# Kernel optimization log

Measured on AMD Instinct MI355X. Metric: run time of the kernel, lower is better.

## Reference

```python
import jax, jax.numpy as jnp
import numpy as np

EMBED_DIM = 1024
N_HEADS = 16
HEAD_DIM = EMBED_DIM // N_HEADS
B, S = 4, 2048


def _rope_tables(seq_len, dim):
    inv_freq = 1.0 / (10000.0 ** (jnp.arange(0, dim, 2, dtype=jnp.float32) / dim))
    freqs = jnp.arange(seq_len, dtype=jnp.float32)[:, None] * inv_freq[None, :]  # [S, dim/2]
    return jnp.cos(freqs), jnp.sin(freqs)


def _apply_rope(x, cos, sin):
    # x: [B, H, S, D]; interleaved-pair complex rotation
    x2 = x.reshape(*x.shape[:-1], HEAD_DIM // 2, 2)
    x0, x1 = x2[..., 0], x2[..., 1]
    c = cos[None, None, :, :]
    s = sin[None, None, :, :]
    r0 = x0 * c - x1 * s
    r1 = x0 * s + x1 * c
    return jnp.stack([r0, r1], axis=-1).reshape(x.shape)


def setup_inputs() -> dict:
    key = jax.random.key(0)
    ks = jax.random.split(key, 8)
    sc = 0.02
    return {
        "query": jax.random.normal(ks[0], (B, S, EMBED_DIM), jnp.float32),
        "key": jax.random.normal(ks[1], (B, S, EMBED_DIM), jnp.float32),
        "value": jax.random.normal(ks[2], (B, S, EMBED_DIM), jnp.float32),
        "Wq": jax.random.normal(ks[3], (EMBED_DIM, EMBED_DIM), jnp.float32) * sc,
        "Wk": jax.random.normal(ks[4], (EMBED_DIM, EMBED_DIM), jnp.float32) * sc,
        "Wv": jax.random.normal(ks[5], (EMBED_DIM, EMBED_DIM), jnp.float32) * sc,
        "Wo": jax.random.normal(ks[6], (EMBED_DIM, EMBED_DIM), jnp.float32) * sc,
        "bo": jnp.zeros((EMBED_DIM,), jnp.float32),
    }


def reference(query, key, value, Wq, Wk, Wv, Wo, bo):
    b, s, _ = query.shape
    # torch nn.Linear: y = x @ W.T
    Q = (query @ Wq.T).reshape(b, s, N_HEADS, HEAD_DIM).transpose(0, 2, 1, 3)
    K = (key @ Wk.T).reshape(b, s, N_HEADS, HEAD_DIM).transpose(0, 2, 1, 3)
    V = (value @ Wv.T).reshape(b, s, N_HEADS, HEAD_DIM).transpose(0, 2, 1, 3)
    cos, sin = _rope_tables(s, HEAD_DIM)
    Q = _apply_rope(Q, cos, sin)
    K = _apply_rope(K, cos, sin)
    scores = jnp.einsum("bhqd,bhkd->bhqk", Q, K) / jnp.sqrt(jnp.float32(HEAD_DIM))
    attn = jax.nn.softmax(scores, axis=-1)
    out = jnp.einsum("bhqk,bhkd->bhqd", attn, V)
    out = out.transpose(0, 2, 1, 3).reshape(b, s, EMBED_DIM)
    return out @ Wo.T + bo
```

## Files before the change

kernel.cpp:

```cpp
#include <hip/hip_runtime.h>
#include <math.h>

typedef __attribute__((ext_vector_type(4))) float f32x4;
typedef __attribute__((ext_vector_type(16))) float f32x16;
typedef __attribute__((ext_vector_type(8))) __bf16 bf16x8;
typedef __attribute__((ext_vector_type(4))) unsigned int u32x4;
typedef __attribute__((ext_vector_type(4))) unsigned short u16x4;

#define DEVI __device__ __forceinline__

constexpr size_t WS_WB  = 0;
constexpr size_t WS_COS = 4ull * 1024 * 1024 * 2;
constexpr size_t WS_SIN = WS_COS + 2048 * 32 * 4;
constexpr size_t WS_QH  = WS_SIN + 2048 * 32 * 4;
constexpr size_t WS_KH  = WS_QH + 64ull * 2048 * 64 * 2;
constexpr size_t WS_VT  = WS_KH + 64ull * 2048 * 64 * 2;
constexpr size_t WS_AO  = WS_VT + 64ull * 64 * 2048 * 2;

DEVI unsigned short f2bf(float x) {
  union { float f; unsigned int u; } v; v.f = x;
  unsigned int r = v.u + 0x7fffu + ((v.u >> 16) & 1u);
  return (unsigned short)(r >> 16);
}

DEVI unsigned cvtpk(float a, float b) {
  union { __bf16 h[2]; unsigned u; } x;
  x.h[0] = (__bf16)a; x.h[1] = (__bf16)b;
  return x.u;
}

DEVI void ld_lds16(const void* g, void* l) {
  __builtin_amdgcn_global_load_lds((const __attribute__((address_space(1))) void*)g,
                                   (__attribute__((address_space(3))) void*)l, 16, 0, 0);
}

__global__ __launch_bounds__(256) void prep(const float* __restrict__ w0,
                                            const float* __restrict__ w1,
                                            const float* __restrict__ w2,
                                            const float* __restrict__ w3,
                                            unsigned short* __restrict__ out,
                                            float* __restrict__ cosT,
                                            float* __restrict__ sinT) {
  if (blockIdx.y == 4) {
    if (blockIdx.x >= 256) return;
    int idx = blockIdx.x * 256 + threadIdx.x;
    int s = idx >> 5, i = idx & 31;
    double ang = (double)s * pow(10000.0, -(double)i / 32.0);
    cosT[idx] = (float)cos(ang);
    sinT[idx] = (float)sin(ang);
    return;
  }
  const float* w = blockIdx.y == 0 ? w0 : blockIdx.y == 1 ? w1 : blockIdx.y == 2 ? w2 : w3;
  int i = (blockIdx.x * 256 + threadIdx.x) * 4;
  f32x4 v = *(const f32x4*)(w + i);
  u16x4 o;
  o.x = f2bf(v.x); o.y = f2bf(v.y); o.z = f2bf(v.z); o.w = f2bf(v.w);
  *(u16x4*)(out + (size_t)blockIdx.y * 1048576 + i) = o;
}

__global__ __launch_bounds__(256) void gemm_qkv(const float* __restrict__ Aq,
                                                const float* __restrict__ Ak,
                                                const float* __restrict__ Av,
                                                const unsigned short* __restrict__ Wb,
                                                unsigned short* __restrict__ Qh,
                                                unsigned short* __restrict__ Kh,
                                                unsigned short* __restrict__ Vt,
                                                const float* __restrict__ cosT,
                                                const float* __restrict__ sinT) {
  __shared__ __align__(16) float AsF[128 * 32];
  __shared__ __align__(16) unsigned short Bs[128 * 32];

  const int mat = blockIdx.y;
  const float* A = mat == 0 ? Aq : mat == 1 ? Ak : Av;
  const unsigned short* W = Wb + (size_t)mat * 1048576;

  const int tid = threadIdx.x;
  const int lane = tid & 63;
  const int wave = tid >> 6;
  const int flat = blockIdx.x;
  const int wgid = (flat & 7) * 64 + (flat >> 3);
  const int m0 = (wgid >> 3) * 128;
  const int n0 = (wgid & 7) * 128;
  const int wm = (wave >> 1) * 64;
  const int wn = (wave & 1) * 64;
  const int hi2 = lane >> 4;

  f32x4 acc[4][4] = {};

  for (int kt = 0; kt < 32; ++kt) {
    const int k0 = kt * 32;
#pragma unroll
    for (int i = 0; i < 4; ++i) {
      int g = i * 256 + tid;
      int row = g >> 3, u = g & 7;
      ld_lds16(A + (size_t)(m0 + row) * 1024 + k0 + ((u ^ (row & 7)) << 2),
               AsF + ((i * 256 + wave * 64) << 2));
    }
#pragma unroll
    for (int i = 0; i < 2; ++i) {
      int g = i * 256 + tid;
      int row = g >> 2, u = g & 3;
      ld_lds16(W + (size_t)(n0 + row) * 1024 + k0 + ((u ^ ((row >> 1) & 3)) << 3),
               Bs + ((i * 256 + wave * 64) << 3));
    }
    __syncthreads();

    bf16x8 af[4], bfr[4];
#pragma unroll
    for (int x = 0; x < 4; ++x) {
      int row = wm + x * 16 + (lane & 15);
      int swz = row & 7;
      f32x4 a0 = *(const f32x4*)(AsF + row * 32 + (((hi2 * 2) ^ swz) << 2));
      f32x4 a1 = *(const f32x4*)(AsF + row * 32 + (((hi2 * 2 + 1) ^ swz) << 2));
      union { u32x4 u; bf16x8 v; } f;
      f.u.x = cvtpk(a0.x, a0.y); f.u.y = cvtpk(a0.z, a0.w);
      f.u.z = cvtpk(a1.x, a1.y); f.u.w = cvtpk(a1.z, a1.w);
      af[x] = f.v;
      int brow = wn + x * 16 + (lane & 15);
      bfr[x] = *(const bf16x8*)(Bs + brow * 32 + ((hi2 ^ ((brow >> 1) & 3)) << 3));
    }
#pragma unroll
    for (int mi = 0; mi < 4; ++mi)
#pragma unroll
      for (int ni = 0; ni < 4; ++ni)
        acc[mi][ni] = __builtin_amdgcn_mfma_f32_16x16x32_bf16(af[mi], bfr[ni], acc[mi][ni], 0, 0, 0);
    __syncthreads();
  }

  const int b = m0 >> 11;
  const int sbase = (m0 & 2047) + wm + ((lane >> 4) << 2);

  if (mat < 2) {
    unsigned short* dst = mat == 0 ? Qh : Kh;
    const float scale = mat == 0 ? 0.18033688011112042f : 1.0f;
#pragma unroll
    for (int ni = 0; ni < 4; ++ni) {
      int n = n0 + wn + ni * 16 + (lane & 15);
      int h = n >> 6, d = n & 63, fi = d >> 1;
      size_t base = (size_t)(b * 16 + h) * 131072 + d;
#pragma unroll
      for (int mi = 0; mi < 4; ++mi) {
#pragma unroll
        for (int r = 0; r < 4; ++r) {
          int s = sbase + mi * 16 + r;
          float v = acc[mi][ni][r];
          float p = __shfl_xor(v, 1);
          float c = cosT[(s << 5) + fi], sn = sinT[(s << 5) + fi];
          float ov = (d & 1) ? (p * sn + v * c) : (v * c - p * sn);
          dst[base + (size_t)s * 64] = f2bf(ov * scale);
        }
      }
    }
  } else {
#pragma unroll
    for (int ni = 0; ni < 4; ++ni) {
      int n = n0 + wn + ni * 16 + (lane & 15);
      int h = n >> 6, d = n & 63;
#pragma unroll
      for (int mi = 0; mi < 4; ++mi) {
        u16x4 pk;
        pk.x = f2bf(acc[mi][ni][0]); pk.y = f2bf(acc[mi][ni][1]);
        pk.z = f2bf(acc[mi][ni][2]); pk.w = f2bf(acc[mi][ni][3]);
        int s = sbase + mi * 16;
        *(u16x4*)(Vt + ((size_t)(b * 16 + h) * 64 + d) * 2048 + s) = pk;
      }
    }
  }
}

__global__ __launch_bounds__(256) void gemm_wo(const unsigned short* __restrict__ Ab,
                                               const unsigned short* __restrict__ W,
                                               float* __restrict__ outp,
                                               const float* __restrict__ bo) {
  __shared__ __align__(16) unsigned short Asb[128 * 32];
  __shared__ __align__(16) unsigned short Bs[128 * 32];

  const int tid = threadIdx.x;
  const int lane = tid & 63;
  const int wave = tid >> 6;
  const int flat = blockIdx.x;
  const int wgid = (flat & 7) * 64 + (flat >> 3);
  const int m0 = (wgid >> 3) * 128;
  const int n0 = (wgid & 7) * 128;
  const int wm = (wave >> 1) * 64;
  const int wn = (wave & 1) * 64;
  const int hi2 = lane >> 4;

  f32x4 acc[4][4] = {};

  for (int kt = 0; kt < 32; ++kt) {
    const int k0 = kt * 32;
#pragma unroll
    for (int i = 0; i < 2; ++i) {
      int g = i * 256 + tid;
      int row = g >> 2, u = g & 3;
      ld_lds16(Ab + (size_t)(m0 + row) * 1024 + k0 + ((u ^ ((row >> 1) & 3)) << 3),
               Asb + ((i * 256 + wave * 64) << 3));
      ld_lds16(W + (size_t)(n0 + row) * 1024 + k0 + ((u ^ ((row >> 1) & 3)) << 3),
               Bs + ((i * 256 + wave * 64) << 3));
    }
    __syncthreads();

    bf16x8 af[4], bfr[4];
#pragma unroll
    for (int x = 0; x < 4; ++x) {
      int row = wm + x * 16 + (lane & 15);
      af[x] = *(const bf16x8*)(Asb + row * 32 + ((hi2 ^ ((row >> 1) & 3)) << 3));
      int brow = wn + x * 16 + (lane & 15);
      bfr[x] = *(const bf16x8*)(Bs + brow * 32 + ((hi2 ^ ((brow >> 1) & 3)) << 3));
    }
#pragma unroll
    for (int mi = 0; mi < 4; ++mi)
#pragma unroll
      for (int ni = 0; ni < 4; ++ni)
        acc[mi][ni] = __builtin_amdgcn_mfma_f32_16x16x32_bf16(af[mi], bfr[ni], acc[mi][ni], 0, 0, 0);
    __syncthreads();
  }

#pragma unroll
  for (int ni = 0; ni < 4; ++ni) {
    int n = n0 + wn + ni * 16 + (lane & 15);
    float bias = bo[n];
#pragma unroll
    for (int mi = 0; mi < 4; ++mi)
#pragma unroll
      for (int r = 0; r < 4; ++r) {
        int m = m0 + wm + mi * 16 + ((lane >> 4) << 2) + r;
        outp[(size_t)m * 1024 + n] = acc[mi][ni][r] + bias;
      }
  }
}

DEVI float tile_sm(f32x16& s0, f32x16& s1, bf16x8* pa) {
  float a0 = 0.f, a1 = 0.f, a2 = 0.f, a3 = 0.f;
#pragma unroll
  for (int r = 0; r < 16; r += 4) {
    s0[r] = __builtin_amdgcn_exp2f(s0[r]);         a0 += s0[r];
    s0[r + 1] = __builtin_amdgcn_exp2f(s0[r + 1]); a1 += s0[r + 1];
    s0[r + 2] = __builtin_amdgcn_exp2f(s0[r + 2]); a2 += s0[r + 2];
    s0[r + 3] = __builtin_amdgcn_exp2f(s0[r + 3]); a3 += s0[r + 3];
  }
#pragma unroll
  for (int r = 0; r < 16; r += 4) {
    s1[r] = __builtin_amdgcn_exp2f(s1[r]);         a0 += s1[r];
    s1[r + 1] = __builtin_amdgcn_exp2f(s1[r + 1]); a1 += s1[r + 1];
    s1[r + 2] = __builtin_amdgcn_exp2f(s1[r + 2]); a2 += s1[r + 2];
    s1[r + 3] = __builtin_amdgcn_exp2f(s1[r + 3]); a3 += s1[r + 3];
  }
#pragma unroll
  for (int blk = 0; blk < 2; ++blk) {
    const f32x16& s = blk ? s1 : s0;
#pragma unroll
    for (int half = 0; half < 2; ++half) {
      int o = half * 8;
      unsigned u0 = cvtpk(s[o + 0], s[o + 1]);
      unsigned u1 = cvtpk(s[o + 2], s[o + 3]);
      unsigned u2 = cvtpk(s[o + 4], s[o + 5]);
      unsigned u3 = cvtpk(s[o + 6], s[o + 7]);
      auto r02 = __builtin_amdgcn_permlane32_swap(u0, u2, false, false);
      auto r13 = __builtin_amdgcn_permlane32_swap(u1, u3, false, false);
      union { u32x4 u; bf16x8 v; } f;
      f.u.x = r02[0]; f.u.y = r13[0]; f.u.z = r02[1]; f.u.w = r13[1];
      pa[blk * 2 + half] = f.v;
    }
  }
  return (a0 + a1) + (a2 + a3);
}

__global__ __launch_bounds__(256, 2) void attn_kernel(const unsigned short* __restrict__ Qh,
                                                      const unsigned short* __restrict__ Kh,
                                                      const unsigned short* __restrict__ Vt,
                                                      unsigned short* __restrict__ AOb) {
  __shared__ __align__(16) unsigned short SM[4][4096];

  const int tid = threadIdx.x, lane = tid & 63, wave = tid >> 6;
  const int lid = blockIdx.x;
  const int xcd = lid & 7, slot = lid >> 3;
  const int bh = xcd * 8 + (slot >> 3);
  const int qb = slot & 7;
  const int q0 = qb * 256 + wave * 64;
  const int lq = lane & 31, hi = lane >> 5;

  const unsigned short* Qgb = Qh + (size_t)bh * 131072;
  const unsigned short* Kgb = Kh + (size_t)bh * 131072;
  const unsigned short* Vgb = Vt + (size_t)bh * 131072;

  bf16x8 qfa[4], qfb[4];
#pragma unroll
  for (int st = 0; st < 4; ++st) {
    qfa[st] = *(const bf16x8*)(Qgb + (size_t)(q0 + lq) * 64 + st * 16 + hi * 8);
    qfb[st] = *(const bf16x8*)(Qgb + (size_t)(q0 + 32 + lq) * 64 + st * 16 + hi * 8);
  }

  const int r0 = wave * 8 + (lane >> 3);
  const int u0 = lane & 7;
  const int sw = (u0 ^ (r0 & 7)) << 3;
  const unsigned short* kp0 = Kgb + r0 * 64 + sw;
  const unsigned short* kp1 = Kgb + (32 + r0) * 64 + sw;
  const unsigned short* vp0 = Vgb + (size_t)r0 * 2048 + sw;
  const unsigned short* vp1 = Vgb + (size_t)(32 + r0) * 2048 + sw;
  const int d0 = wave * 512, d1 = 2048 + wave * 512;

  auto stage = [&](int buf, int kt) {
    unsigned short* Kd = SM[buf * 2];
    unsigned short* Vd = SM[buf * 2 + 1];
    ld_lds16(kp0 + kt * 4096, Kd + d0);
    ld_lds16(kp1 + kt * 4096, Kd + d1);
    ld_lds16(vp0 + kt * 64, Vd + d0);
    ld_lds16(vp1 + kt * 64, Vd + d1);
  };
  auto frag = [&](const unsigned short* base, int row, int c) -> bf16x8 {
    return *(const bf16x8*)(base + row * 64 + (((c ^ (row & 7)) << 3)));
  };

  f32x16 o0a = {}, o1a = {}, o0b = {}, o1b = {};
  float lsA = 0.f, lsB = 0.f;

  stage(0, 0);

  for (int kt = 0; kt < 32; ++kt) {
    const int cur = kt & 1;
    if (kt < 31) {
      stage(cur ^ 1, kt + 1);
      asm volatile("s_waitcnt vmcnt(4)" ::: "memory");
    } else {
      asm volatile("s_waitcnt vmcnt(0)" ::: "memory");
    }
    __builtin_amdgcn_s_barrier();
    const unsigned short* Kc = SM[cur * 2];
    const unsigned short* Vc = SM[cur * 2 + 1];

    bf16x8 kf0[4], kf1[4], vf0[4], vf1[4];
#pragma unroll
    for (int st = 0; st < 4; ++st) {
      kf0[st] = frag(Kc, lq, st * 2 + hi);
      kf1[st] = frag(Kc, 32 + lq, st * 2 + hi);
      vf0[st] = frag(Vc, lq, st * 2 + hi);
      vf1[st] = frag(Vc, 32 + lq, st * 2 + hi);
    }

    f32x16 s0a = {}, s1a = {}, s0b = {}, s1b = {};
#pragma unroll
    for (int st = 0; st < 4; ++st) {
      s0a = __builtin_amdgcn_mfma_f32_32x32x16_bf16(kf0[st], qfa[st], s0a, 0, 0, 0);
      s1a = __builtin_amdgcn_mfma_f32_32x32x16_bf16(kf1[st], qfa[st], s1a, 0, 0, 0);
      s0b = __builtin_amdgcn_mfma_f32_32x32x16_bf16(kf0[st], qfb[st], s0b, 0, 0, 0);
      s1b = __builtin_amdgcn_mfma_f32_32x32x16_bf16(kf1[st], qfb[st], s1b, 0, 0, 0);
    }

    bf16x8 paA[4], paB[4];
    lsA += tile_sm(s0a, s1a, paA);
    lsB += tile_sm(s0b, s1b, paB);

#pragma unroll
    for (int kc = 0; kc < 4; ++kc) {
      o0a = __builtin_amdgcn_mfma_f32_32x32x16_bf16(paA[kc], vf0[kc], o0a, 0, 0, 0);
      o1a = __builtin_amdgcn_mfma_f32_32x32x16_bf16(paA[kc], vf1[kc], o1a, 0, 0, 0);
      o0b = __builtin_amdgcn_mfma_f32_32x32x16_bf16(paB[kc], vf0[kc], o0b, 0, 0, 0);
      o1b = __builtin_amdgcn_mfma_f32_32x32x16_bf16(paB[kc], vf1[kc], o1b, 0, 0, 0);
    }

    if (kt < 31) {
      __builtin_amdgcn_s_barrier();
    }
  }

  lsA += __shfl_xor(lsA, 32);
  lsB += __shfl_xor(lsB, 32);
  const int b = bh >> 4, h = bh & 15;
#pragma unroll
  for (int r = 0; r < 16; ++r) {
    int row = (r & 3) + 8 * (r >> 2) + 4 * hi;
    float ia = 1.0f / __shfl(lsA, row);
    float ib = 1.0f / __shfl(lsB, row);
    unsigned short* da = AOb + (size_t)(b * 2048 + q0 + row) * 1024 + h * 64;
    unsigned short* db = AOb + (size_t)(b * 2048 + q0 + 32 + row) * 1024 + h * 64;
    da[lq] = f2bf(o0a[r] * ia);
    da[32 + lq] = f2bf(o1a[r] * ia);
    db[lq] = f2bf(o0b[r] * ib);
    db[32 + lq] = f2bf(o1b[r] * ib);
  }
}

extern "C" void kernel_launch(void* const* d_in, const int* in_sizes, int n_in,
                              void* d_out, int out_size, void* d_ws, size_t ws_size,
                              hipStream_t stream) {
  const float* query = (const float*)d_in[0];
  const float* key = (const float*)d_in[1];
  const float* value = (const float*)d_in[2];
  const float* Wq = (const float*)d_in[3];
  const float* Wk = (const float*)d_in[4];
  const float* Wv = (const float*)d_in[5];
  const float* Wo = (const float*)d_in[6];
  const float* bo = (const float*)d_in[7];

  char* ws = (char*)d_ws;
  unsigned short* Wb = (unsigned short*)(ws + WS_WB);
  float* cosT = (float*)(ws + WS_COS);
  float* sinT = (float*)(ws + WS_SIN);
  unsigned short* Qh = (unsigned short*)(ws + WS_QH);
  unsigned short* Kh = (unsigned short*)(ws + WS_KH);
  unsigned short* Vt = (unsigned short*)(ws + WS_VT);
  unsigned short* AOb = (unsigned short*)(ws + WS_AO);

  prep<<<dim3(1024, 5), 256, 0, stream>>>(Wq, Wk, Wv, Wo, Wb, cosT, sinT);
  gemm_qkv<<<dim3(512, 3), 256, 0, stream>>>(query, key, value, Wb, Qh, Kh, Vt, cosT, sinT);
  attn_kernel<<<512, 256, 0, stream>>>(Qh, Kh, Vt, AOb);
  gemm_wo<<<512, 256, 0, stream>>>(AOb, Wb + 3145728, (float*)d_out, bo);
}
```

Measured before the change: 216.4 us.

## Double-buffer LDS tiles in QKV GEMM to overlap loads with MFMA

Splits the A and B shared-memory tiles in the fused QKV projection GEMM into two buffers. The global-to-LDS loads for the next k-tile are issued after the current fragments are read and before the MFMAs run, so memory latency overlaps compute. This replaces two syncthreads per iteration with one waitcnt plus a barrier. LDS use doubles to roughly 48KB per block, which may lower occupancy.

```diff
diff --git a/kernel.cpp b/kernel.cpp
--- a/kernel.cpp
+++ b/kernel.cpp
@@ -67,8 +67,10 @@
                                                 unsigned short* __restrict__ Vt,
                                                 const float* __restrict__ cosT,
                                                 const float* __restrict__ sinT) {
-  __shared__ __align__(16) float AsF[128 * 32];
-  __shared__ __align__(16) unsigned short Bs[128 * 32];
+  __shared__ __align__(16) float As0[128 * 32];
+  __shared__ __align__(16) float As1[128 * 32];
+  __shared__ __align__(16) unsigned short Bs0[128 * 32];
+  __shared__ __align__(16) unsigned short Bs1[128 * 32];
 
   const int mat = blockIdx.y;
   const float* A = mat == 0 ? Aq : mat == 1 ? Ak : Av;
@@ -87,44 +89,57 @@
 
   f32x4 acc[4][4] = {};
 
-  for (int kt = 0; kt < 32; ++kt) {
+  auto stage = [&](float* AsD, unsigned short* BsD, int kt) {
     const int k0 = kt * 32;
 #pragma unroll
     for (int i = 0; i < 4; ++i) {
       int g = i * 256 + tid;
       int row = g >> 3, u = g & 7;
       ld_lds16(A + (size_t)(m0 + row) * 1024 + k0 + ((u ^ (row & 7)) << 2),
-               AsF + ((i * 256 + wave * 64) << 2));
+               AsD + ((i * 256 + wave * 64) << 2));
     }
 #pragma unroll
     for (int i = 0; i < 2; ++i) {
       int g = i * 256 + tid;
       int row = g >> 2, u = g & 3;
       ld_lds16(W + (size_t)(n0 + row) * 1024 + k0 + ((u ^ ((row >> 1) & 3)) << 3),
-               Bs + ((i * 256 + wave * 64) << 3));
-    }
-    __syncthreads();
-
+               BsD + ((i * 256 + wave * 64) << 3));
+    }
+  };
+
+  auto round = [&](const float* AsC, const unsigned short* BsC, int nkt,
+                   float* AsN, unsigned short* BsN) {
     bf16x8 af[4], bfr[4];
 #pragma unroll
     for (int x = 0; x < 4; ++x) {
       int row = wm + x * 16 + (lane & 15);
       int swz = row & 7;
-      f32x4 a0 = *(const f32x4*)(AsF + row * 32 + (((hi2 * 2) ^ swz) << 2));
-      f32x4 a1 = *(const f32x4*)(AsF + row * 32 + (((hi2 * 2 + 1) ^ swz) << 2));
+      f32x4 a0 = *(const f32x4*)(AsC + row * 32 + (((hi2 * 2) ^ swz) << 2));
+      f32x4 a1 = *(const f32x4*)(AsC + row * 32 + (((hi2 * 2 + 1) ^ swz) << 2));
       union { u32x4 u; bf16x8 v; } f;
       f.u.x = cvtpk(a0.x, a0.y); f.u.y = cvtpk(a0.z, a0.w);
       f.u.z = cvtpk(a1.x, a1.y); f.u.w = cvtpk(a1.z, a1.w);
       af[x] = f.v;
       int brow = wn + x * 16 + (lane & 15);
-      bfr[x] = *(const bf16x8*)(Bs + brow * 32 + ((hi2 ^ ((brow >> 1) & 3)) << 3));
-    }
+      bfr[x] = *(const bf16x8*)(BsC + brow * 32 + ((hi2 ^ ((brow >> 1) & 3)) << 3));
+    }
+    if (nkt < 32) stage(AsN, BsN, nkt);
 #pragma unroll
     for (int mi = 0; mi < 4; ++mi)
 #pragma unroll
       for (int ni = 0; ni < 4; ++ni)
         acc[mi][ni] = __builtin_amdgcn_mfma_f32_16x16x32_bf16(af[mi], bfr[ni], acc[mi][ni], 0, 0, 0);
-    __syncthreads();
+    asm volatile("s_waitcnt vmcnt(0)" ::: "memory");
+    __builtin_amdgcn_s_barrier();
+  };
+
+  stage(As0, Bs0, 0);
+  asm volatile("s_waitcnt vmcnt(0)" ::: "memory");
+  __builtin_amdgcn_s_barrier();
+
+  for (int kt = 0; kt < 32; kt += 2) {
+    round(As0, Bs0, kt + 1, As1, Bs1);
+    round(As1, Bs1, kt + 2, As0, Bs0);
   }
 
   const int b = m0 >> 11;
```

Result: faster. 205.4 us (-5.1%).
